# Performance work log

Hardware: AMD Instinct MI355X
Metric: run time of the kernel (lower is better)

The kernel has to match this reference:

```python
import jax, jax.numpy as jnp
import numpy as np


def _cayley(X):
    # torch orthogonal parametrization, orthogonal_map='cayley', use_trivialization=False:
    # A = tril(X,-1); A = A - A^T (skew);  Q = (I - A/2)^{-1} (I + A/2)
    n = X.shape[0]
    A = jnp.tril(X, -1)
    A = A - A.T
    I = jnp.eye(n, dtype=X.dtype)
    return jnp.linalg.solve(I - 0.5 * A, I + 0.5 * A)


def setup_inputs() -> dict:
    key = jax.random.key(0)
    ks = jax.random.split(key, 8)
    L, R = 64, 64
    B, S = 4, 2048
    x = jax.random.normal(ks[0], (B, S, L * R), dtype=jnp.float32)
    return {
        "x": x,
        "u_left": jax.random.normal(ks[1], (L, L), dtype=jnp.float32) * 0.02,
        "v_left": jax.random.normal(ks[2], (L, L), dtype=jnp.float32) * 0.02,
        "diag_left": jnp.ones((L,), dtype=jnp.float32),
        "u_right": jax.random.normal(ks[3], (R, R), dtype=jnp.float32) * 0.02,
        "v_right": jax.random.normal(ks[4], (R, R), dtype=jnp.float32) * 0.02,
        "diag_right": jnp.ones((R,), dtype=jnp.float32),
        "diag_scale": 1.0 + 0.01 * jax.random.normal(ks[5], (L * R,), dtype=jnp.float32),
    }


def reference(x, u_left, v_left, diag_left, u_right, v_right, diag_right, diag_scale):
    L = diag_left.shape[0]
    R = diag_right.shape[0]
    # SVD-composed trans matrices: M = Cayley(U) @ diag(S) @ Cayley(V)
    m_left = _cayley(u_left) @ (diag_left[:, None] * _cayley(v_left))    # [L, L]
    m_right = _cayley(u_right) @ (diag_right[:, None] * _cayley(v_right))  # [R, R]
    # add_diag: elementwise diagonal scale on hidden dim
    xs = x * diag_scale
    shp = xs.shape
    xm = xs.reshape(-1, L, R)  # [N, L, R]
    # kronecker_matmul: m_left^T @ X @ m_right
    out = jnp.einsum('il,nij,jr->nlr', m_left, xm, m_right)
    return out.reshape(shp)
```

## Files before the change

### kernel.cpp

```cpp
#include <hip/hip_runtime.h>
#include <hip/hip_bf16.h>

typedef __attribute__((ext_vector_type(8))) short short8;
typedef __attribute__((ext_vector_type(4))) short short4v;
typedef __attribute__((ext_vector_type(4))) float floatx4;

#define MFMA(a, b, c) __builtin_amdgcn_mfma_f32_16x16x32_bf16((a), (b), (c), 0, 0, 0)

__device__ __forceinline__ short f2bf(float f) {
    unsigned u = __float_as_uint(f);
    u += 0x7fffu + ((u >> 16) & 1u);
    return (short)(u >> 16);
}

__device__ __forceinline__ short8 pack_bf16(floatx4 a, floatx4 b) {
    short8 r;
    r[0] = f2bf(a.x); r[1] = f2bf(a.y); r[2] = f2bf(a.z); r[3] = f2bf(a.w);
    r[4] = f2bf(b.x); r[5] = f2bf(b.y); r[6] = f2bf(b.z); r[7] = f2bf(b.w);
    return r;
}

__device__ void cayley64(const float* __restrict__ X, const float* __restrict__ dg,
                         short* outArr, int mode,
                         short* Brow, float* Bcol, short* T0, short* T1, int tid)
{
    int i0 = (tid * 16) >> 6;
    int j0 = (tid * 16) & 63;
#pragma unroll
    for (int s = 0; s < 16; ++s) {
        int i = i0, j = j0 + s;
        float b = 0.f;
        if (i > j)      b =  0.5f * X[i * 64 + j];
        else if (i < j) b = -0.5f * X[j * 64 + i];
        Brow[i * 72 + j] = f2bf(b);
        Bcol[j * 68 + i] = b;
        T0[j * 72 + i]   = f2bf(b);
    }
    __syncthreads();

    int lane = tid & 63, w = tid >> 6, m = lane & 15, q = lane >> 4;
    int arow = (w * 16 + m) * 72;
    short8 a0 = *(const short8*)&Brow[arow + q * 8];
    short8 a1 = *(const short8*)&Brow[arow + 32 + q * 8];

    short* Tbuf[2] = {T0, T1};
    int cur = 0;
    const int NSTEP = 6;
    for (int step = 0; step < NSTEP; ++step) {
        bool last = (step == NSTEP - 1);
        short* Tr = Tbuf[cur];
        short* Tw = Tbuf[cur ^ 1];
#pragma unroll
        for (int c = 0; c < 4; ++c) {
            int coff = c * 16 + m;
            short8 b0 = *(const short8*)&Tr[coff * 72 + q * 8];
            short8 b1 = *(const short8*)&Tr[coff * 72 + 32 + q * 8];
            floatx4 acc = {0.f, 0.f, 0.f, 0.f};
            acc = MFMA(a0, b0, acc);
            acc = MFMA(a1, b1, acc);
            int row0 = w * 16 + q * 4;
            floatx4 badd = *(const floatx4*)&Bcol[coff * 68 + row0];
            floatx4 t = badd + acc;
            if (!last) {
                short4v pk = { f2bf(t.x), f2bf(t.y), f2bf(t.z), f2bf(t.w) };
                *(short4v*)&Tw[coff * 72 + row0] = pk;
            } else {
                int col = coff;
                floatx4 cv;
                cv.x = ((row0 + 0) == col ? 1.f : 0.f) + 2.f * t.x;
                cv.y = ((row0 + 1) == col ? 1.f : 0.f) + 2.f * t.y;
                cv.z = ((row0 + 2) == col ? 1.f : 0.f) + 2.f * t.z;
                cv.w = ((row0 + 3) == col ? 1.f : 0.f) + 2.f * t.w;
                if (mode == 0) {
                    outArr[(row0 + 0) * 72 + col] = f2bf(cv.x);
                    outArr[(row0 + 1) * 72 + col] = f2bf(cv.y);
                    outArr[(row0 + 2) * 72 + col] = f2bf(cv.z);
                    outArr[(row0 + 3) * 72 + col] = f2bf(cv.w);
                } else {
                    floatx4 dv = *(const floatx4*)&dg[row0];
                    short4v pk = { f2bf(cv.x * dv.x), f2bf(cv.y * dv.y),
                                   f2bf(cv.z * dv.z), f2bf(cv.w * dv.w) };
                    *(short4v*)&outArr[col * 72 + row0] = pk;
                }
            }
        }
        __syncthreads();
        cur ^= 1;
    }
}

__global__ __launch_bounds__(256) void k_prep(
        const float* __restrict__ u_l, const float* __restrict__ v_l, const float* __restrict__ dg_l,
        const float* __restrict__ u_r, const float* __restrict__ v_r, const float* __restrict__ dg_r,
        short* __restrict__ wsOut)
{
    __shared__ __align__(16) short Brow[64 * 72];
    __shared__ __align__(16) float Bcol[64 * 68];
    __shared__ __align__(16) short T0[64 * 72];
    __shared__ __align__(16) short T1[64 * 72];
    __shared__ __align__(16) short CvA[64 * 72];
    __shared__ __align__(16) short CuB[64 * 72];

    int tid = threadIdx.x;
    const float* U  = (blockIdx.x == 0) ? u_l  : u_r;
    const float* V  = (blockIdx.x == 0) ? v_l  : v_r;
    const float* DG = (blockIdx.x == 0) ? dg_l : dg_r;
    short* outT = wsOut + blockIdx.x * 4096;

    cayley64(V, DG, CvA, 1, Brow, Bcol, T0, T1, tid);
    __syncthreads();
    cayley64(U, DG, CuB, 0, Brow, Bcol, T0, T1, tid);
    __syncthreads();

    int lane = tid & 63, w = tid >> 6, m = lane & 15, q = lane >> 4;
    int arow = (w * 16 + m) * 72;
    short8 a0 = *(const short8*)&CvA[arow + q * 8];
    short8 a1 = *(const short8*)&CvA[arow + 32 + q * 8];
#pragma unroll
    for (int c = 0; c < 4; ++c) {
        short8 b0 = *(const short8*)&CuB[(c * 16 + m) * 72 + q * 8];
        short8 b1 = *(const short8*)&CuB[(c * 16 + m) * 72 + 32 + q * 8];
        floatx4 acc = {0.f, 0.f, 0.f, 0.f};
        acc = MFMA(a0, b0, acc);
        acc = MFMA(a1, b1, acc);
        int row0 = w * 16 + q * 4, col = c * 16 + m;
        outT[(row0 + 0) * 64 + col] = f2bf(acc.x);
        outT[(row0 + 1) * 64 + col] = f2bf(acc.y);
        outT[(row0 + 2) * 64 + col] = f2bf(acc.z);
        outT[(row0 + 3) * 64 + col] = f2bf(acc.w);
    }
}

#define WPW 2

__global__ __launch_bounds__(256, 2) void k_main(
        const float* __restrict__ x, const float* __restrict__ dsc,
        const short* __restrict__ mLT, const short* __restrict__ mRT,
        float* __restrict__ out, int N)
{
    __shared__ __align__(16) short STb[4][2][16 * 72];

    int tid = threadIdx.x, lane = tid & 63, w = tid >> 6;
    int m = lane & 15, q = lane >> 4;
    const int fragoff = q * 8;

    short8 qf[4][2], pfB[4][2];
#pragma unroll
    for (int c = 0; c < 4; ++c) {
        qf[c][0] = *(const short8*)&mRT[(c * 16 + m) * 64 + fragoff];
        qf[c][1] = *(const short8*)&mRT[(c * 16 + m) * 64 + 32 + fragoff];
    }
#pragma unroll
    for (int r = 0; r < 4; ++r) {
        pfB[r][0] = *(const short8*)&mLT[(r * 16 + m) * 64 + fragoff];
        pfB[r][1] = *(const short8*)&mLT[(r * 16 + m) * 64 + 32 + fragoff];
    }

    const int wid = blockIdx.x * 4 + w;

#pragma unroll
    for (int i = 0; i < WPW; ++i) {
        int n = wid * WPW + i;
        if (n >= N) break;
        const float* xp = x + (size_t)n * 4096;
        float* op = out + (size_t)n * 4096;

        floatx4 xf[4][4];
#pragma unroll
        for (int r = 0; r < 4; ++r) {
            const float* rp = xp + (r * 16 + m) * 64 + fragoff;
            xf[r][0] = *(const floatx4*)&rp[0];
            xf[r][1] = *(const floatx4*)&rp[4];
            xf[r][2] = *(const floatx4*)&rp[32];
            xf[r][3] = *(const floatx4*)&rp[36];
        }

        short8 xa[4][2];
#pragma unroll
        for (int r = 0; r < 4; ++r) {
            const float* dp = dsc + (r * 16 + m) * 64 + fragoff;
            floatx4 d0 = *(const floatx4*)&dp[0];
            floatx4 d1 = *(const floatx4*)&dp[4];
            floatx4 d2 = *(const floatx4*)&dp[32];
            floatx4 d3 = *(const floatx4*)&dp[36];
            xa[r][0] = pack_bf16(xf[r][0] * d0, xf[r][1] * d1);
            xa[r][1] = pack_bf16(xf[r][2] * d2, xf[r][3] * d3);
        }

#pragma unroll
        for (int c = 0; c < 4; ++c) {
            short* stc = &STb[w][c & 1][0];
#pragma unroll
            for (int r = 0; r < 4; ++r) {
                floatx4 s = {0.f, 0.f, 0.f, 0.f};
                s = MFMA(xa[r][0], qf[c][0], s);
                s = MFMA(xa[r][1], qf[c][1], s);
                short4v pk = { f2bf(s.x), f2bf(s.y), f2bf(s.z), f2bf(s.w) };
                *(short4v*)&stc[m * 72 + r * 16 + q * 4] = pk;
            }
            short8 sb0 = *(const short8*)&stc[m * 72 + fragoff];
            short8 sb1 = *(const short8*)&stc[m * 72 + 32 + fragoff];
#pragma unroll
            for (int r = 0; r < 4; ++r) {
                floatx4 o = {0.f, 0.f, 0.f, 0.f};
                o = MFMA(sb0, pfB[r][0], o);
                o = MFMA(sb1, pfB[r][1], o);
                *(floatx4*)&op[(r * 16 + m) * 64 + c * 16 + q * 4] = o;
            }
        }
    }
}

extern "C" void kernel_launch(void* const* d_in, const int* in_sizes, int n_in,
                              void* d_out, int out_size, void* d_ws, size_t ws_size,
                              hipStream_t stream) {
    const float* x    = (const float*)d_in[0];
    const float* u_l  = (const float*)d_in[1];
    const float* v_l  = (const float*)d_in[2];
    const float* dg_l = (const float*)d_in[3];
    const float* u_r  = (const float*)d_in[4];
    const float* v_r  = (const float*)d_in[5];
    const float* dg_r = (const float*)d_in[6];
    const float* dsc  = (const float*)d_in[7];
    float* out = (float*)d_out;
    short* ws  = (short*)d_ws;

    int N = in_sizes[0] / 4096;

    hipLaunchKernelGGL(k_prep, dim3(2), dim3(256), 0, stream,
                       u_l, v_l, dg_l, u_r, v_r, dg_r, ws);
    int grid = (N + 4 * WPW - 1) / (4 * WPW);
    hipLaunchKernelGGL(k_main, dim3(grid), dim3(256), 0, stream,
                       x, dsc, ws, ws + 4096, out, N);
}
```

Before: 277.7 us.

## Coalesce x loads and output stores via LDS staging and prefetch next matrix

The kernel now loads each 64x64 input matrix with fully coalesced 16-byte-per-lane row-contiguous reads and restages it through LDS into the MFMA fragment layout. Outputs go through an LDS buffer so that global stores are contiguous. The diag_scale vector is cached once per block in LDS, and the next matrix's x is prefetched into registers while the current one is computed. The goal is better global memory coalescing on this bandwidth-bound kernel, at the cost of more LDS traffic, higher LDS usage and extra registers (16 more floatx4 for the prefetch), which may lower occupancy.

```diff
diff --git a/kernel.cpp b/kernel.cpp
--- a/kernel.cpp
+++ b/kernel.cpp
@@ -138,12 +138,21 @@
         const short* __restrict__ mLT, const short* __restrict__ mRT,
         float* __restrict__ out, int N)
 {
-    __shared__ __align__(16) short STb[4][2][16 * 72];
+    __shared__ __align__(16) float DS[4096];
+    __shared__ __align__(16) short Xa[4][64 * 72];
+    __shared__ __align__(16) short ST[4][16 * 72];
+    __shared__ __align__(16) float Oq[4][16 * 68];
 
     int tid = threadIdx.x, lane = tid & 63, w = tid >> 6;
     int m = lane & 15, q = lane >> 4;
     const int fragoff = q * 8;
 
+#pragma unroll
+    for (int j = 0; j < 4; ++j) {
+        int e = (j * 256 + tid) * 4;
+        *(floatx4*)&DS[e] = *(const floatx4*)&dsc[e];
+    }
+
     short8 qf[4][2], pfB[4][2];
 #pragma unroll
     for (int c = 0; c < 4; ++c) {
@@ -155,58 +164,86 @@
         pfB[r][0] = *(const short8*)&mLT[(r * 16 + m) * 64 + fragoff];
         pfB[r][1] = *(const short8*)&mLT[(r * 16 + m) * 64 + 32 + fragoff];
     }
+    __syncthreads();
+
+    short* xa_lds = &Xa[w][0];
+    short* st_lds = &ST[w][0];
+    float* oq_lds = &Oq[w][0];
 
     const int wid = blockIdx.x * 4 + w;
-
-#pragma unroll
-    for (int i = 0; i < WPW; ++i) {
-        int n = wid * WPW + i;
+    const int n0 = wid * WPW;
+
+    floatx4 xv[16];
+    if (n0 < N) {
+        const float* xp = x + (size_t)n0 * 4096 + lane * 4;
+#pragma unroll
+        for (int j = 0; j < 16; ++j) xv[j] = *(const floatx4*)&xp[j * 256];
+    }
+
+#pragma unroll
+    for (int it = 0; it < WPW; ++it) {
+        int n = n0 + it;
         if (n >= N) break;
-        const float* xp = x + (size_t)n * 4096;
-        float* op = out + (size_t)n * 4096;
-
-        floatx4 xf[4][4];
+
+#pragma unroll
+        for (int j = 0; j < 16; ++j) {
+            floatx4 dv = *(const floatx4*)&DS[j * 256 + lane * 4];
+            floatx4 v = xv[j] * dv;
+            short4v pk = { f2bf(v.x), f2bf(v.y), f2bf(v.z), f2bf(v.w) };
+            *(short4v*)&xa_lds[((lane >> 4) + j * 4) * 72 + (lane & 15) * 4] = pk;
+        }
+
+        floatx4 nxv[16];
+        bool pfn = (it + 1 < WPW) && (n + 1 < N);
+        if (pfn) {
+            const float* xp = x + (size_t)(n + 1) * 4096 + lane * 4;
+#pragma unroll
+            for (int j = 0; j < 16; ++j) nxv[j] = *(const floatx4*)&xp[j * 256];
+        }
+
+        short8 xaf[4][2];
 #pragma unroll
         for (int r = 0; r < 4; ++r) {
-            const float* rp = xp + (r * 16 + m) * 64 + fragoff;
-            xf[r][0] = *(const floatx4*)&rp[0];
-            xf[r][1] = *(const floatx4*)&rp[4];
-            xf[r][2] = *(const floatx4*)&rp[32];
-            xf[r][3] = *(const floatx4*)&rp[36];
-        }
-
-        short8 xa[4][2];
-#pragma unroll
-        for (int r = 0; r < 4; ++r) {
-            const float* dp = dsc + (r * 16 + m) * 64 + fragoff;
-            floatx4 d0 = *(const floatx4*)&dp[0];
-            floatx4 d1 = *(const floatx4*)&dp[4];
-            floatx4 d2 = *(const floatx4*)&dp[32];
-            floatx4 d3 = *(const floatx4*)&dp[36];
-            xa[r][0] = pack_bf16(xf[r][0] * d0, xf[r][1] * d1);
-            xa[r][1] = pack_bf16(xf[r][2] * d2, xf[r][3] * d3);
-        }
-
+            xaf[r][0] = *(const short8*)&xa_lds[(r * 16 + m) * 72 + fragoff];
+            xaf[r][1] = *(const short8*)&xa_lds[(r * 16 + m) * 72 + 32 + fragoff];
+        }
+
+        short8 sb[4][2];
 #pragma unroll
         for (int c = 0; c < 4; ++c) {
-            short* stc = &STb[w][c & 1][0];
 #pragma unroll
             for (int r = 0; r < 4; ++r) {
                 floatx4 s = {0.f, 0.f, 0.f, 0.f};
-                s = MFMA(xa[r][0], qf[c][0], s);
-                s = MFMA(xa[r][1], qf[c][1], s);
+                s = MFMA(xaf[r][0], qf[c][0], s);
+                s = MFMA(xaf[r][1], qf[c][1], s);
                 short4v pk = { f2bf(s.x), f2bf(s.y), f2bf(s.z), f2bf(s.w) };
-                *(short4v*)&stc[m * 72 + r * 16 + q * 4] = pk;
-            }
-            short8 sb0 = *(const short8*)&stc[m * 72 + fragoff];
-            short8 sb1 = *(const short8*)&stc[m * 72 + 32 + fragoff];
-#pragma unroll
-            for (int r = 0; r < 4; ++r) {
+                *(short4v*)&st_lds[m * 72 + r * 16 + q * 4] = pk;
+            }
+            sb[c][0] = *(const short8*)&st_lds[m * 72 + fragoff];
+            sb[c][1] = *(const short8*)&st_lds[m * 72 + 32 + fragoff];
+        }
+
+        float* op = out + (size_t)n * 4096;
+#pragma unroll
+        for (int r = 0; r < 4; ++r) {
+#pragma unroll
+            for (int c = 0; c < 4; ++c) {
                 floatx4 o = {0.f, 0.f, 0.f, 0.f};
-                o = MFMA(sb0, pfB[r][0], o);
-                o = MFMA(sb1, pfB[r][1], o);
-                *(floatx4*)&op[(r * 16 + m) * 64 + c * 16 + q * 4] = o;
-            }
+                o = MFMA(sb[c][0], pfB[r][0], o);
+                o = MFMA(sb[c][1], pfB[r][1], o);
+                *(floatx4*)&oq_lds[m * 68 + c * 16 + q * 4] = o;
+            }
+#pragma unroll
+            for (int j = 0; j < 4; ++j) {
+                int row = (lane >> 4) + j * 4, col = (lane & 15) * 4;
+                floatx4 v = *(const floatx4*)&oq_lds[row * 68 + col];
+                *(floatx4*)&op[r * 1024 + j * 256 + lane * 4] = v;
+            }
+        }
+
+        if (pfn) {
+#pragma unroll
+            for (int j = 0; j < 16; ++j) xv[j] = nxv[j];
         }
     }
 }
```

Measured after the change: 270.1 us. 2.7% less time.
